# Kernel tuning notes

Hardware: AMD Instinct MI355X
Metric: run time of the kernel (lower is better)

The kernel has to match this reference:

```python
import jax, jax.numpy as jnp
import numpy as np

ISQRT2 = 0.7071067811865476  # 1/sqrt(2), haar analysis/synthesis coefficient
LEVELS = 13                  # pywt.dwt_max_level(8192, 'haar') = log2(8192)
J = 4                        # recursion_limit
BN_EPS = 1e-5


def haar_wavedec(x, levels):
    """Full-depth haar DWT (mode='zero' is exact for power-of-2 length).
    x: [..., N]. Returns bank [cA_L, cD_L, cD_{L-1}, ..., cD_1] (pywt order).
    Vectorized over batch AND channel dims at once (the per-channel python
    loop in the torch module computes identical math per channel)."""
    a = x
    details = []
    for _ in range(levels):
        even, odd = a[..., ::2], a[..., 1::2]
        details.append((even - odd) * ISQRT2)
        a = (even + odd) * ISQRT2
    return [a] + details[::-1]


def haar_waverec(bank):
    """Inverse of haar_wavedec; bank in pywt order [cA, cD_coarse..cD_fine]."""
    a = bank[0]
    for d in bank[1:]:
        up = jnp.stack([a + d, a - d], axis=-1) * ISQRT2  # interleave even/odd
        a = up.reshape(a.shape[:-1] + (a.shape[-1] * 2,))
    return a


def batch_norm_train(y, g, b):
    # BatchNorm1d training mode: stats over (batch, length) per channel, biased var
    mean = jnp.mean(y, axis=(0, 2), keepdims=True)
    var = jnp.var(y, axis=(0, 2), keepdims=True)
    return (y - mean) * jax.lax.rsqrt(var + BN_EPS) * g[None, :, None] + b[None, :, None]


def reference(x, gamma, beta):
    # x: [B, C, N]; gamma, beta: [J, C]
    bank = haar_wavedec(x, LEVELS)  # computed once, reused for all masks
    zeros_bank = [jnp.zeros_like(c) for c in bank]

    # masked_inputs[j]: IWT keeping only band j (pool_inputs=False -> full bank)
    masked_inputs = []
    for j in range(J):
        mb = [bank[i] if i == j else zeros_bank[i] for i in range(len(bank))]
        masked_inputs.append(haar_waverec(mb))

    # masked_targets[j]: IWT keeping bands 0..j (pool_targets=False)
    masked_targets = []
    for j in range(J):
        mb = [bank[i] if i <= j else zeros_bank[i] for i in range(len(bank))]
        masked_targets.append(haar_waverec(mb))

    # per-level BatchNorm on inputs only
    masked_inputs = [batch_norm_train(masked_inputs[j], gamma[j], beta[j]) for j in range(J)]

    # stack for a single output tensor: [2, J, B, C, N]
    return jnp.stack([jnp.stack(masked_inputs), jnp.stack(masked_targets)])


def setup_inputs() -> dict:
    key = jax.random.key(0)
    x = jax.random.normal(key, (64, 16, 8192), dtype=jnp.float32)
    gamma = jnp.ones((J, 16), dtype=jnp.float32)
    beta = jnp.zeros((J, 16), dtype=jnp.float32)
    return {"x": x, "gamma": gamma, "beta": beta}
```

## Files before the change

kernel.cpp:

```cpp
#include <hip/hip_runtime.h>


#define STATS_STRIDE 16

typedef float f32x4 __attribute__((ext_vector_type(4)));

__global__ __launch_bounds__(256) void stats_targets_kernel(const float* __restrict__ x,
                                                            float* __restrict__ stats,
                                                            f32x4* __restrict__ out) {
    int row = blockIdx.x;
    int t = threadIdx.x;
    const f32x4* xr = reinterpret_cast<const f32x4*>(x) + (size_t)row * 2048;
    float s[8];
#pragma unroll
    for (int k = 0; k < 8; ++k) {
        f32x4 v = __builtin_nontemporal_load(&xr[t + 256 * k]);
        s[k] = (v.x + v.y) + (v.z + v.w);
    }
    __shared__ float red[8][4];
    __shared__ float sb[16];
    int lane = t & 63, wave = t >> 6;
#pragma unroll
    for (int k = 0; k < 8; ++k) {
        float v = s[k];
#pragma unroll
        for (int off = 32; off; off >>= 1) v += __shfl_down(v, off, 64);
        if (lane == 0) red[k][wave] = v;
    }
    __syncthreads();
    if (t < 8) sb[7 + t] = (red[t][0] + red[t][1] + red[t][2] + red[t][3]) * (1.0f / 1024.0f);
    __syncthreads();
    if (t == 0) {
        float m2[4], m1[2];
#pragma unroll
        for (int k = 0; k < 4; ++k) m2[k] = 0.5f * (sb[7 + 2 * k] + sb[7 + 2 * k + 1]);
        m1[0] = 0.5f * (m2[0] + m2[1]);
        m1[1] = 0.5f * (m2[2] + m2[3]);
        sb[0] = 0.5f * (m1[0] + m1[1]);
        sb[1] = m1[0]; sb[2] = m1[1];
        sb[3] = m2[0]; sb[4] = m2[1]; sb[5] = m2[2]; sb[6] = m2[3];
    }
    __syncthreads();
    if (t < 15) stats[(size_t)row * STATS_STRIDE + t] = sb[t];
    float rv[15];
#pragma unroll
    for (int k = 0; k < 15; ++k) rv[k] = sb[k];
#pragma unroll
    for (int j = 0; j < 4; ++j) {
        f32x4* orow = out + ((size_t)(4 + j) * 1024 + row) * 2048;
        int sh = 3 - j;
#pragma unroll
        for (int i = 0; i < 8; ++i) {
            float v = rv[(1 << j) - 1 + (i >> sh)];
            f32x4 q = {v, v, v, v};
            orow[t + (i << 8)] = q;
        }
    }
}

__global__ __launch_bounds__(256) void inputs_kernel(const float* __restrict__ stats,
                                                     const float* __restrict__ gamma,
                                                     const float* __restrict__ beta,
                                                     f32x4* __restrict__ out) {
    int blk = blockIdx.x;
    int j = blk >> 8;
    int c = (blk >> 4) & 15;
    int bg = blk & 15;
    int t = threadIdx.x;
    __shared__ float ss[2];
    if (t < 64) {
        const float* s = stats + (size_t)((t << 4) + c) * STATS_STRIDE;
        float sum = 0.f, sum2 = 0.f;
        float B = (float)(8192 >> j);
        if (j == 0) {
            float d = s[0];
            sum = d; sum2 = d * d;
        } else {
            int base = (1 << j) - 1, pb = (1 << (j - 1)) - 1;
            for (int k = 0; k < (1 << j); ++k) {
                float d = s[base + k] - s[pb + (k >> 1)];
                sum += d; sum2 += d * d;
            }
        }
        sum *= B; sum2 *= B;
#pragma unroll
        for (int off = 32; off; off >>= 1) {
            sum  += __shfl_down(sum, off, 64);
            sum2 += __shfl_down(sum2, off, 64);
        }
        if (t == 0) {
            const float N = 64.0f * 8192.0f;
            float mean = sum / N;
            float var = sum2 / N - mean * mean;
            float inv = rsqrtf(var + 1e-5f);
            float sc = gamma[(j << 4) + c] * inv;
            ss[0] = sc;
            ss[1] = beta[(j << 4) + c] - mean * sc;
        }
    }
    __syncthreads();
    float sc = ss[0], sh0 = ss[1];
    int shr = 3 - j;
#pragma unroll
    for (int bb = 0; bb < 4; ++bb) {
        int row = (((bg << 2) + bb) << 4) + c;
        const float* s = stats + (size_t)row * STATS_STRIDE;
        float rv[8];
#pragma unroll
        for (int r = 0; r < 8; ++r) {
            int run = (r < (1 << j)) ? r : 0;
            float mj = s[(1 << j) - 1 + run];
            float d = (j == 0) ? mj : mj - s[(1 << (j - 1)) - 1 + (run >> 1)];
            rv[r] = d * sc + sh0;
        }
        f32x4* orow = out + ((size_t)j * 1024 + row) * 2048;
#pragma unroll
        for (int i = 0; i < 8; ++i) {
            float v = rv[i >> shr];
            f32x4 q = {v, v, v, v};
            orow[t + (i << 8)] = q;
        }
    }
}

extern "C" void kernel_launch(void* const* d_in, const int* in_sizes, int n_in,
                              void* d_out, int out_size, void* d_ws, size_t ws_size,
                              hipStream_t stream) {
    const float* x     = (const float*)d_in[0];
    const float* gamma = (const float*)d_in[1];
    const float* beta  = (const float*)d_in[2];
    f32x4* out = (f32x4*)d_out;
    float* stats = (float*)d_ws;

    stats_targets_kernel<<<1024, 256, 0, stream>>>(x, stats, out);
    inputs_kernel<<<1024, 256, 0, stream>>>(stats, gamma, beta, out);
}
```

Measured before the change: 53.10 us.

## Fuse stats and inputs kernels into one cooperative kernel with grid sync

Merges the two launches into a single cooperative kernel that computes per-row block means, writes the target outputs, then uses a grid-wide sync before each block computes BatchNorm scale/shift for its channel (one wave per level) and writes the normalized input outputs from register-held stats. This removes a kernel launch and the re-reading of per-row stats. In exchange, every block redundantly computes the per-channel BN reduction, and the grid barrier needs all 1024 blocks co-resident, which cooperative launch must guarantee on this device.

```diff
diff --git a/kernel.cpp b/kernel.cpp
--- a/kernel.cpp
+++ b/kernel.cpp
@@ -1,15 +1,23 @@
 #include <hip/hip_runtime.h>
+#include <hip/hip_cooperative_groups.h>
+
+namespace cg = cooperative_groups;
 
 
 #define STATS_STRIDE 16
 
 typedef float f32x4 __attribute__((ext_vector_type(4)));
 
-__global__ __launch_bounds__(256) void stats_targets_kernel(const float* __restrict__ x,
-                                                            float* __restrict__ stats,
-                                                            f32x4* __restrict__ out) {
+__global__ __launch_bounds__(256) void fused_kernel(const float* __restrict__ x,
+                                                    const float* __restrict__ gamma,
+                                                    const float* __restrict__ beta,
+                                                    float* __restrict__ stats,
+                                                    f32x4* __restrict__ out) {
     int row = blockIdx.x;
+    int c = row & 15;
     int t = threadIdx.x;
+    int lane = t & 63, wave = t >> 6;
+
     const f32x4* xr = reinterpret_cast<const f32x4*>(x) + (size_t)row * 2048;
     float s[8];
 #pragma unroll
@@ -19,7 +27,6 @@
     }
     __shared__ float red[8][4];
     __shared__ float sb[16];
-    int lane = t & 63, wave = t >> 6;
 #pragma unroll
     for (int k = 0; k < 8; ++k) {
         float v = s[k];
@@ -45,6 +52,43 @@
     float rv[15];
 #pragma unroll
     for (int k = 0; k < 15; ++k) rv[k] = sb[k];
+
+    cg::this_grid().sync();
+
+    __shared__ float ss[4][2];
+    {
+        int j = wave;
+        const float* sp = stats + (size_t)((lane << 4) + c) * STATS_STRIDE;
+        float sum = 0.f, sum2 = 0.f;
+        if (j == 0) {
+            float d = sp[0];
+            sum = d; sum2 = d * d;
+        } else {
+            int base = (1 << j) - 1, pb = (1 << (j - 1)) - 1;
+            for (int k = 0; k < (1 << j); ++k) {
+                float d = sp[base + k] - sp[pb + (k >> 1)];
+                sum += d; sum2 += d * d;
+            }
+        }
+        float B = (float)(8192 >> j);
+        sum *= B; sum2 *= B;
+#pragma unroll
+        for (int off = 32; off; off >>= 1) {
+            sum  += __shfl_down(sum, off, 64);
+            sum2 += __shfl_down(sum2, off, 64);
+        }
+        if (lane == 0) {
+            const float N = 64.0f * 8192.0f;
+            float mean = sum / N;
+            float var = sum2 / N - mean * mean;
+            float inv = rsqrtf(var + 1e-5f);
+            float sc = gamma[(j << 4) + c] * inv;
+            ss[j][0] = sc;
+            ss[j][1] = beta[(j << 4) + c] - mean * sc;
+        }
+    }
+    __syncthreads();
+
 #pragma unroll
     for (int j = 0; j < 4; ++j) {
         f32x4* orow = out + ((size_t)(4 + j) * 1024 + row) * 2048;
@@ -56,67 +100,17 @@
             orow[t + (i << 8)] = q;
         }
     }
-}
-
-__global__ __launch_bounds__(256) void inputs_kernel(const float* __restrict__ stats,
-                                                     const float* __restrict__ gamma,
-                                                     const float* __restrict__ beta,
-                                                     f32x4* __restrict__ out) {
-    int blk = blockIdx.x;
-    int j = blk >> 8;
-    int c = (blk >> 4) & 15;
-    int bg = blk & 15;
-    int t = threadIdx.x;
-    __shared__ float ss[2];
-    if (t < 64) {
-        const float* s = stats + (size_t)((t << 4) + c) * STATS_STRIDE;
-        float sum = 0.f, sum2 = 0.f;
-        float B = (float)(8192 >> j);
-        if (j == 0) {
-            float d = s[0];
-            sum = d; sum2 = d * d;
-        } else {
-            int base = (1 << j) - 1, pb = (1 << (j - 1)) - 1;
-            for (int k = 0; k < (1 << j); ++k) {
-                float d = s[base + k] - s[pb + (k >> 1)];
-                sum += d; sum2 += d * d;
-            }
-        }
-        sum *= B; sum2 *= B;
 #pragma unroll
-        for (int off = 32; off; off >>= 1) {
-            sum  += __shfl_down(sum, off, 64);
-            sum2 += __shfl_down(sum2, off, 64);
-        }
-        if (t == 0) {
-            const float N = 64.0f * 8192.0f;
-            float mean = sum / N;
-            float var = sum2 / N - mean * mean;
-            float inv = rsqrtf(var + 1e-5f);
-            float sc = gamma[(j << 4) + c] * inv;
-            ss[0] = sc;
-            ss[1] = beta[(j << 4) + c] - mean * sc;
-        }
-    }
-    __syncthreads();
-    float sc = ss[0], sh0 = ss[1];
-    int shr = 3 - j;
-#pragma unroll
-    for (int bb = 0; bb < 4; ++bb) {
-        int row = (((bg << 2) + bb) << 4) + c;
-        const float* s = stats + (size_t)row * STATS_STRIDE;
-        float rv[8];
-#pragma unroll
-        for (int r = 0; r < 8; ++r) {
-            int run = (r < (1 << j)) ? r : 0;
-            float mj = s[(1 << j) - 1 + run];
-            float d = (j == 0) ? mj : mj - s[(1 << (j - 1)) - 1 + (run >> 1)];
-            rv[r] = d * sc + sh0;
-        }
+    for (int j = 0; j < 4; ++j) {
+        float sc = ss[j][0], sh0 = ss[j][1];
+        int shr = 3 - j;
         f32x4* orow = out + ((size_t)j * 1024 + row) * 2048;
 #pragma unroll
         for (int i = 0; i < 8; ++i) {
-            float v = rv[i >> shr];
+            int run = i >> shr;
+            float mj = rv[(1 << j) - 1 + run];
+            float d = (j == 0) ? mj : mj - rv[(1 << (j - 1)) - 1 + (run >> 1)];
+            float v = d * sc + sh0;
             f32x4 q = {v, v, v, v};
             orow[t + (i << 8)] = q;
         }
@@ -132,6 +126,6 @@
     f32x4* out = (f32x4*)d_out;
     float* stats = (float*)d_ws;
 
-    stats_targets_kernel<<<1024, 256, 0, stream>>>(x, stats, out);
-    inputs_kernel<<<1024, 256, 0, stream>>>(stats, gamma, beta, out);
+    void* args[] = {(void*)&x, (void*)&gamma, (void*)&beta, (void*)&stats, (void*)&out};
+    hipLaunchCooperativeKernel((const void*)fused_kernel, dim3(1024), dim3(256), args, 0, stream);
 }
```

Measured after the change: 130.7 us. 146% more time.
